# Kernel tuning notes

Measured on AMD Instinct MI355X. Metric: run time of the kernel, lower is better.

The kernel has to match this reference:

```python
import jax, jax.numpy as jnp
import numpy as np

B, L, D, H = 2, 2048, 2048, 16
HD = D // H          # head_dim = 128
LD = HD // 4         # latent_dim = 32


def _linear_params(key, fan_in, fan_out):
    kw, kb = jax.random.split(key)
    bound = 1.0 / np.sqrt(fan_in)
    W = jax.random.uniform(kw, (fan_in, fan_out), jnp.float32, -bound, bound)
    b = jax.random.uniform(kb, (fan_out,), jnp.float32, -bound, bound)
    return W, b


def setup_inputs() -> dict:
    key = jax.random.key(0)
    ks = jax.random.split(key, 12)
    x = jax.random.normal(ks[0], (B, L, D), jnp.float32)
    cos = jax.random.uniform(ks[1], (L, HD // 2), jnp.float32)
    sin = jax.random.uniform(ks[2], (L, HD // 2), jnp.float32)
    Wq, bq = _linear_params(ks[3], D, D)
    Wk, bk = _linear_params(ks[4], D, D)
    Wv, bv = _linear_params(ks[5], D, D)
    Wqc, bqc = _linear_params(ks[6], HD, LD)
    Wkc, bkc = _linear_params(ks[7], HD, LD)
    Wvc, bvc = _linear_params(ks[8], HD, LD)
    Wd, bd = _linear_params(ks[9], LD, HD)
    Wo, bo = _linear_params(ks[10], D, D)
    return dict(x=x, cos=cos, sin=sin, Wq=Wq, bq=bq, Wk=Wk, bk=bk, Wv=Wv, bv=bv,
                Wqc=Wqc, bqc=bqc, Wkc=Wkc, bkc=bkc, Wvc=Wvc, bvc=bvc,
                Wd=Wd, bd=bd, Wo=Wo, bo=bo)


def _apply_rope(q, k, cos, sin):
    # q, k: (B, H, L, HD); cos, sin: (L, HD//2) -> broadcast over B, H
    c = cos[None, None, :, :]
    s = sin[None, None, :, :]
    qe, qo = q[..., ::2], q[..., 1::2]
    ke, ko = k[..., ::2], k[..., 1::2]
    q_rot = jnp.stack([qe * c - qo * s, qe * s + qo * c], axis=-1).reshape(q.shape)
    k_rot = jnp.stack([ke * c - ko * s, ke * s + ko * c], axis=-1).reshape(k.shape)
    return q_rot, k_rot


def reference(x, cos, sin, Wq, bq, Wk, bk, Wv, bv,
              Wqc, bqc, Wkc, bkc, Wvc, bvc, Wd, bd, Wo, bo):
    b, l, d = x.shape
    # projections -> (B, H, L, HD)
    q = (x @ Wq + bq).reshape(b, l, H, HD).transpose(0, 2, 1, 3)
    k = (x @ Wk + bk).reshape(b, l, H, HD).transpose(0, 2, 1, 3)
    v = (x @ Wv + bv).reshape(b, l, H, HD).transpose(0, 2, 1, 3)
    q, k = _apply_rope(q, k, cos, sin)
    # low-rank compression into latent_dim
    qc = jnp.einsum('bhld,de->bhle', q, Wqc) + bqc
    kc = jnp.einsum('bhld,de->bhle', k, Wkc) + bkc
    vc = jnp.einsum('bhld,de->bhle', v, Wvc) + bvc
    scores = jnp.einsum('bhqe,bhke->bhqk', qc, kc) / np.sqrt(LD).astype(np.float32)
    causal = jnp.tril(jnp.ones((l, l), dtype=bool))  # True = keep
    scores = jnp.where(causal[None, None], scores, -jnp.inf)
    probs = jax.nn.softmax(scores, axis=-1)
    attn = jnp.einsum('bhqk,bhke->bhqe', probs, vc)
    attn = jnp.einsum('bhle,ed->bhld', attn, Wd) + bd  # decompress to HD
    attn = attn.transpose(0, 2, 1, 3).reshape(b, l, d)
    return attn @ Wo + bo
```

## Files before the change

### kernel.cpp

```cpp
#include <hip/hip_runtime.h>
#include <hip/hip_bf16.h>


#define Bsz 2
#define Lseq 2048
#define Dmod 2048
#define Hn 16
#define HDim 128
#define LDim 32

typedef __bf16 bf16x8 __attribute__((ext_vector_type(8)));
typedef float f32x4 __attribute__((ext_vector_type(4)));
typedef __hip_bfloat16 bf16;

#define GLDS16(g, l)                                                    \
  __builtin_amdgcn_global_load_lds(                                     \
      (const __attribute__((address_space(1))) unsigned int*)(g),       \
      (__attribute__((address_space(3))) unsigned int*)(l), 16, 0, 0)

#define SM_COS 0
#define SM_SIN 131072
#define SM_WC 262144
#define SM_BC 274432
#define SM_WD 274528
#define SM_BD 278624
#define SM_BO 278752
#define SM_BQKV 280800
#define SM_TOT 286944

__global__ void detect_dtype(const ushort* __restrict__ x, int* __restrict__ flag) {
  int t = threadIdx.x;
  int bad = 0;
  for (int k = 0; k < 4; ++k) {
    ushort u = x[t * 4 + k];
    int ex = (u >> 7) & 0xFF;
    if (ex >= 0xC0) bad = 1;
  }
  unsigned long long b = __ballot(bad);
  if (t == 0) *flag = (b != 0ULL) ? 1 : 0;
}

__device__ inline void conv8(const void* src, size_t so, bf16* dst, size_t dof, int f32) {
  if (f32) {
    const float* s = (const float*)src + so;
    bf16 tmp[8] __attribute__((aligned(16)));
    for (int j = 0; j < 8; ++j) tmp[j] = __float2bfloat16(s[j]);
    *(uint4*)&dst[dof] = *(uint4*)tmp;
  } else {
    *(uint4*)&dst[dof] = *(const uint4*)((const ushort*)src + so);
  }
}

__device__ inline float cv1(const void* s, size_t i, int f32) {
  return f32 ? ((const float*)s)[i] : __bfloat162float(((const bf16*)s)[i]);
}

#define NB_T3 3072
#define NB_WV 2048
#define NB_CX 4096
#define NB_PREP 160
#define NB_FBP 256
#define NB_PREP_ALL (NB_T3 + NB_WV + NB_CX + NB_PREP + NB_FBP)

__global__ __launch_bounds__(256) void prep_all(
    const void* xS, const void* cosS, const void* sinS, const void* WqS,
    const void* WkS, const void* WvS, const void* WoS, const void* WqcS,
    const void* WkcS, const void* WvcS, const void* bqcS, const void* bkcS,
    const void* bvcS, const void* WdS, const void* bdS, const void* boS,
    const void* bqS, const void* bkS, const void* bvS,
    bf16* __restrict__ xb, bf16* __restrict__ WvB, bf16* __restrict__ WtQK,
    bf16* __restrict__ WtO, bf16* __restrict__ small, bf16* __restrict__ wctG,
    bf16* __restrict__ wdtG, float* __restrict__ bo_part,
    const int* __restrict__ flagp) {
  __shared__ __align__(16) char shm[16640];
  int f32 = *flagp;
  int blk = blockIdx.x;
  int t = threadIdx.x;

  if (blk < NB_T3) {
    float (*tile)[65] = (float(*)[65])shm;
    int z = blk >> 10, rem = blk & 1023;
    const void* W = (z == 0) ? WqS : (z == 1) ? WkS : WoS;
    bf16* Wt = (z == 2) ? WtO : (WtQK + (size_t)z * 2048 * 2048);
    int n0 = (rem & 31) * 64, k0 = (rem >> 5) * 64;
    int x = (t & 7) * 8, y = t >> 3;
    for (int p = 0; p < 2; ++p) {
      int r = y + p * 32;
      if (f32) {
        const float* src = (const float*)W + (size_t)(k0 + r) * 2048 + n0 + x;
        float4 a = *(const float4*)src;
        float4 b2 = *(const float4*)(src + 4);
        tile[r][x + 0] = a.x; tile[r][x + 1] = a.y; tile[r][x + 2] = a.z; tile[r][x + 3] = a.w;
        tile[r][x + 4] = b2.x; tile[r][x + 5] = b2.y; tile[r][x + 6] = b2.z; tile[r][x + 7] = b2.w;
      } else {
        const ushort* src = (const ushort*)W + (size_t)(k0 + r) * 2048 + n0 + x;
        uint4 u = *(const uint4*)src;
        bf16* e = (bf16*)&u;
        for (int jj = 0; jj < 8; ++jj) tile[r][x + jj] = __bfloat162float(e[jj]);
      }
    }
    __syncthreads();
    for (int p = 0; p < 2; ++p) {
      int n = y + p * 32;
      bf16 tmp[8] __attribute__((aligned(16)));
      for (int jj = 0; jj < 8; ++jj) tmp[jj] = __float2bfloat16(tile[x + jj][n]);
      *(uint4*)&Wt[(size_t)(n0 + n) * 2048 + k0 + x] = *(uint4*)tmp;
    }
  } else if (blk < NB_T3 + NB_WV) {
    size_t e = ((size_t)(blk - NB_T3) * 256 + t) * 8;
    conv8(WvS, e, WvB, e, f32);
  } else if (blk < NB_T3 + NB_WV + NB_CX) {
    size_t e = ((size_t)(blk - NB_T3 - NB_WV) * 256 + t) * 8;
    conv8(xS, e, xb, e, f32);
  } else if (blk < NB_T3 + NB_WV + NB_CX + NB_PREP) {
    int tid = (blk - NB_T3 - NB_WV - NB_CX) * 256 + t;
    if (tid < SM_TOT / 8) {
      size_t e = (size_t)tid * 8;
      const void* src;
      size_t so;
      if (e < SM_SIN) { src = cosS; so = e - SM_COS; }
      else if (e < SM_WC) { src = sinS; so = e - SM_SIN; }
      else if (e < SM_BC) { size_t r = e - SM_WC; src = (r < 4096) ? WqcS : (r < 8192) ? WkcS : WvcS; so = r & 4095; }
      else if (e < SM_WD) { size_t r = e - SM_BC; src = (r < 32) ? bqcS : (r < 64) ? bkcS : bvcS; so = r & 31; }
      else if (e < SM_BD) { src = WdS; so = e - SM_WD; }
      else if (e < SM_BO) { src = bdS; so = e - SM_BD; }
      else if (e < SM_BQKV) { src = boS; so = e - SM_BO; }
      else { size_t r = e - SM_BQKV; src = (r < 2048) ? bqS : (r < 4096) ? bkS : bvS; so = r & 2047; }
      conv8(src, so, small, e, f32);
    } else {
      int idx = tid - SM_TOT / 8;
      for (int i = idx; i < 16384; i += 40960 - SM_TOT / 8) {
        if (i < 12288) {
          int reg = i >> 12, rem2 = i & 4095, n = rem2 >> 7, k = rem2 & 127;
          const void* src = (reg == 0) ? WqcS : (reg == 1) ? WkcS : WvcS;
          wctG[i] = __float2bfloat16(cv1(src, (size_t)k * 32 + n, f32));
        } else {
          int i2 = i - 12288, o = i2 >> 5, e = i2 & 31;
          wdtG[i2] = __float2bfloat16(cv1(WdS, (size_t)e * 128 + o, f32));
        }
      }
    }
  } else {
    float* red = (float*)shm;
    int rem = blk - (NB_T3 + NB_WV + NB_CX + NB_PREP);
    int nb = rem & 15, kb = rem >> 4;
    int col = nb * 128 + (t & 127);
    int half = t >> 7;
    float s = 0.f;
    int kbase = kb * 128 + half * 64;
    for (int i = 0; i < 64; ++i) {
      int k = kbase + i;
      s += cv1(bdS, k & 127, f32) * cv1(WoS, (size_t)k * 2048 + col, f32);
    }
    red[t] = s;
    __syncthreads();
    if (half == 0) bo_part[kb * 2048 + col] = red[t] + red[t + 128];
  }
}

__global__ __launch_bounds__(256) void fold_all(
    const bf16* __restrict__ WvB, const bf16* __restrict__ wctG,
    const bf16* __restrict__ WtO, const bf16* __restrict__ small,
    const void* boS, const float* __restrict__ bo_part, const void* bvS,
    const void* bvcS, const void* WvcS, bf16* __restrict__ Wvt,
    bf16* __restrict__ Wot, float* __restrict__ boF, float* __restrict__ bvF,
    const int* __restrict__ flagp) {
  int blk = blockIdx.x;
  int t = threadIdx.x, lane = t & 63, w = t >> 6;
  int qd = lane >> 4, ln = lane & 15;
  if (blk < 256) {
    int nb = blk & 15, h = blk >> 4;
    f32x4 acc[2][2] = {};
    for (int kt = 0; kt < 4; ++kt) {
      bf16x8 af[2], bfr[2];
      for (int i = 0; i < 2; ++i)
        af[i] = *(const bf16x8*)&wctG[8192 + (i * 16 + ln) * 128 + kt * 32 + qd * 8];
      for (int j = 0; j < 2; ++j)
        bfr[j] = *(const bf16x8*)&WvB[(size_t)(nb * 128 + w * 32 + j * 16 + ln) * 2048 +
                                      h * 128 + kt * 32 + qd * 8];
      for (int i = 0; i < 2; ++i)
        for (int j = 0; j < 2; ++j)
          acc[i][j] = __builtin_amdgcn_mfma_f32_16x16x32_bf16(af[i], bfr[j], acc[i][j], 0, 0, 0);
    }
    for (int i = 0; i < 2; ++i)
      for (int j = 0; j < 2; ++j)
        for (int r = 0; r < 4; ++r) {
          int e = i * 16 + qd * 4 + r;
          int col = nb * 128 + w * 32 + j * 16 + ln;
          Wvt[(size_t)(h * 32 + e) * 2048 + col] = __float2bfloat16(acc[i][j][r]);
        }
  } else if (blk < 512) {
    int rem = blk - 256;
    int mb = rem & 15, h = rem >> 4;
    f32x4 acc[2][2] = {};
    for (int kt = 0; kt < 4; ++kt) {
      bf16x8 af[2], bfr[2];
      for (int i = 0; i < 2; ++i)
        af[i] = *(const bf16x8*)&WtO[(size_t)(mb * 128 + w * 32 + i * 16 + ln) * 2048 +
                                     h * 128 + kt * 32 + qd * 8];
      for (int j = 0; j < 2; ++j)
        bfr[j] = *(const bf16x8*)&small[SM_WD + (j * 16 + ln) * 128 + kt * 32 + qd * 8];
      for (int i = 0; i < 2; ++i)
        for (int j = 0; j < 2; ++j)
          acc[i][j] = __builtin_amdgcn_mfma_f32_16x16x32_bf16(af[i], bfr[j], acc[i][j], 0, 0, 0);
    }
    for (int i = 0; i < 2; ++i)
      for (int j = 0; j < 2; ++j)
        for (int r = 0; r < 4; ++r) {
          int row = mb * 128 + w * 32 + i * 16 + qd * 4 + r;
          int col = h * 32 + j * 16 + ln;
          Wot[(size_t)row * 512 + col] = __float2bfloat16(acc[i][j][r]);
        }
  } else {
    int f32 = *flagp;
    int tid = (blk - 512) * 256 + t;
    if (tid < 2048) {
      float s = cv1(boS, tid, f32);
      for (int kb = 0; kb < 16; ++kb) s += bo_part[kb * 2048 + tid];
      boF[tid] = s;
    } else if (tid < 2560) {
      int j = tid - 2048, h = j >> 5, e = j & 31;
      float s = cv1(bvcS, e, f32);
      for (int hd = 0; hd < 128; ++hd)
        s += cv1(bvS, h * 128 + hd, f32) * cv1(WvcS, (size_t)hd * 32 + e, f32);
      bvF[j] = s;
    }
  }
}

#define ESTR 136
__global__ __launch_bounds__(256) void gemm_qk_compress(
    const bf16* __restrict__ A, const bf16* __restrict__ Bt,
    const bf16* __restrict__ small, const bf16* __restrict__ wctG,
    bf16* __restrict__ qc, bf16* __restrict__ kc) {
  __shared__ bf16 sh[128 * ESTR];
  bf16* lA = sh;
  bf16* lB = sh + 4096;
  const int K = 2048;
  int id = blockIdx.x;
  int lg = (id & 7) * 128 + (id >> 3);
  int bm = lg >> 5, bn = lg & 31;
  int reg = bn >> 4, h = bn & 15;
  int t = threadIdx.x;
  int lane = t & 63, w = t >> 6;
  int wm = (w >> 1) * 64, wn = (w & 1) * 64;
  int qd = lane >> 4, ln = lane & 15;

  f32x4 acc[4][4] = {};
  const bf16* Ab = A + (size_t)(bm * 128) * K;
  const bf16* Bb = Bt + (size_t)(bn * 128) * K;

  for (int kt = 0; kt < K; kt += 32) {
    for (int p = 0; p < 2; ++p) {
      int slot = t + p * 256;
      int r = slot >> 2, c = (slot & 3) * 8;
      GLDS16(&Ab[(size_t)r * K + kt + c], &lA[slot * 8]);
      GLDS16(&Bb[(size_t)r * K + kt + c], &lB[slot * 8]);
    }
    __syncthreads();
    bf16x8 af[4], bfr[4];
    for (int i = 0; i < 4; ++i) af[i] = *(bf16x8*)&lA[(wm + i * 16 + ln) * 32 + qd * 8];
    for (int j = 0; j < 4; ++j) bfr[j] = *(bf16x8*)&lB[(wn + j * 16 + ln) * 32 + qd * 8];
    for (int i = 0; i < 4; ++i)
      for (int j = 0; j < 4; ++j)
        acc[i][j] = __builtin_amdgcn_mfma_f32_16x16x32_bf16(af[i], bfr[j], acc[i][j], 0, 0, 0);
    __syncthreads();
  }

  for (int j = 0; j < 4; ++j) {
    int col = wn + j * 16 + ln;
    float bv = __bfloat162float(small[SM_BQKV + bn * 128 + col]);
    for (int i = 0; i < 4; ++i)
      for (int r = 0; r < 4; ++r)
        sh[(wm + i * 16 + qd * 4 + r) * ESTR + col] = __float2bfloat16(acc[i][j][r] + bv);
  }
  __syncthreads();

  int r0 = w * 32;
  int b = bm >> 4;
  int bh = b * Hn + h;
  bf16x8 bfr2[2][4];
  for (int nt = 0; nt < 2; ++nt)
    for (int kt = 0; kt < 4; ++kt)
      bfr2[nt][kt] = *(const bf16x8*)&wctG[reg * 4096 + (nt * 16 + ln) * 128 + kt * 32 + qd * 8];
  float bc[2];
  bc[0] = __bfloat162float(small[SM_BC + reg * 32 + ln]);
  bc[1] = __bfloat162float(small[SM_BC + reg * 32 + 16 + ln]);

  for (int mt = 0; mt < 2; ++mt) {
    int lb = r0 + mt * 16 + ln;
    int lg2 = (bm & 15) * 128 + lb;
    f32x4 c2[2] = {};
    for (int kt = 0; kt < 4; ++kt) {
      uint4 u = *(uint4*)&sh[lb * ESTR + kt * 32 + qd * 8];
      bf16* e8 = (bf16*)&u;
      int pbase = kt * 16 + qd * 4;
      for (int j = 0; j < 4; ++j) {
        float cvv = __bfloat162float(small[SM_COS + (size_t)lg2 * 64 + pbase + j]);
        float svv = __bfloat162float(small[SM_SIN + (size_t)lg2 * 64 + pbase + j]);
        float ev = __bfloat162float(e8[2 * j]);
        float ov = __bfloat162float(e8[2 * j + 1]);
        e8[2 * j] = __float2bfloat16(ev * cvv - ov * svv);
        e8[2 * j + 1] = __float2bfloat16(ev * svv + ov * cvv);
      }
      bf16x8 a = *(bf16x8*)&u;
      c2[0] = __builtin_amdgcn_mfma_f32_16x16x32_bf16(a, bfr2[0][kt], c2[0], 0, 0, 0);
      c2[1] = __builtin_amdgcn_mfma_f32_16x16x32_bf16(a, bfr2[1][kt], c2[1], 0, 0, 0);
    }
    int lgbase = (bm & 15) * 128 + r0 + mt * 16 + qd * 4;
    bf16* dst = (reg == 0) ? qc : kc;
    for (int nt = 0; nt < 2; ++nt)
      for (int r = 0; r < 4; ++r)
        dst[((size_t)bh * Lseq + lgbase + r) * 32 + nt * 16 + ln] =
            __float2bfloat16(c2[nt][r] + bc[nt]);
  }
}

__global__ __launch_bounds__(256) void gemm_v_fold(const bf16* __restrict__ A,
                                                   const bf16* __restrict__ Wvt,
                                                   const float* __restrict__ bvF,
                                                   bf16* __restrict__ vcT) {
  __shared__ bf16 lA[64 * 32];
  __shared__ bf16 lB[64 * 32];
  const int K = 2048;
  int bm = blockIdx.y, nb = blockIdx.x;
  int t = threadIdx.x;
  int lane = t & 63, w = t >> 6;
  int wm = (w >> 1) * 32, wn = (w & 1) * 32;
  int qd = lane >> 4, ln = lane & 15;

  f32x4 acc[2][2] = {};
  const bf16* Ab = A + (size_t)(bm * 64) * K;
  const bf16* Bb = Wvt + (size_t)(nb * 64) * K;

  int r = t >> 2, c = (t & 3) * 8;
  for (int kt = 0; kt < K; kt += 32) {
    GLDS16(&Ab[(size_t)r * K + kt + c], &lA[t * 8]);
    GLDS16(&Bb[(size_t)r * K + kt + c], &lB[t * 8]);
    __syncthreads();
    bf16x8 af[2], bfr[2];
    for (int i = 0; i < 2; ++i) af[i] = *(bf16x8*)&lA[(wm + i * 16 + ln) * 32 + qd * 8];
    for (int j = 0; j < 2; ++j) bfr[j] = *(bf16x8*)&lB[(wn + j * 16 + ln) * 32 + qd * 8];
    for (int i = 0; i < 2; ++i)
      for (int j = 0; j < 2; ++j)
        acc[i][j] = __builtin_amdgcn_mfma_f32_16x16x32_bf16(af[i], bfr[j], acc[i][j], 0, 0, 0);
    __syncthreads();
  }

  int b = bm >> 5;
  for (int j = 0; j < 2; ++j) {
    int n = nb * 64 + wn + j * 16 + ln;
    float bb = bvF[n];
    for (int i = 0; i < 2; ++i) {
      int lloc = (bm & 31) * 64 + wm + i * 16 + qd * 4;
      bf16 p4[4] __attribute__((aligned(8)));
      for (int rr = 0; rr < 4; ++rr) p4[rr] = __float2bfloat16(acc[i][j][rr] + bb);
      *(uint2*)&vcT[((size_t)(b * 512 + n)) * 2048 + lloc] = *(uint2*)p4;
    }
  }
}

__global__ __launch_bounds__(256) void gemm_bias_out(const bf16* __restrict__ A,
                                                     const bf16* __restrict__ Bt,
                                                     const float* __restrict__ bias,
                                                     void* __restrict__ C,
                                                     int M, int N, int K,
                                                     const int* __restrict__ flagp) {
  __shared__ bf16 lA[128 * 32];
  __shared__ bf16 lB[128 * 32];
  int f32out = *flagp;
  int bm = blockIdx.y, bn = blockIdx.x;
  int t = threadIdx.x;
  int lane = t & 63, w = t >> 6;
  int wm = (w >> 1) * 64, wn = (w & 1) * 64;
  int qd = lane >> 4, ln = lane & 15;

  f32x4 acc[4][4] = {};
  const bf16* Ab = A + (size_t)(bm * 128) * K;
  const bf16* Bb = Bt + (size_t)(bn * 128) * K;

  for (int kt = 0; kt < K; kt += 32) {
    for (int p = 0; p < 2; ++p) {
      int slot = t + p * 256;
      int r = slot >> 2, c = (slot & 3) * 8;
      GLDS16(&Ab[(size_t)r * K + kt + c], &lA[slot * 8]);
      GLDS16(&Bb[(size_t)r * K + kt + c], &lB[slot * 8]);
    }
    __syncthreads();
    bf16x8 af[4], bfr[4];
    for (int i = 0; i < 4; ++i) af[i] = *(bf16x8*)&lA[(wm + i * 16 + ln) * 32 + qd * 8];
    for (int j = 0; j < 4; ++j) bfr[j] = *(bf16x8*)&lB[(wn + j * 16 + ln) * 32 + qd * 8];
    for (int i = 0; i < 4; ++i)
      for (int j = 0; j < 4; ++j)
        acc[i][j] = __builtin_amdgcn_mfma_f32_16x16x32_bf16(af[i], bfr[j], acc[i][j], 0, 0, 0);
    __syncthreads();
  }
  for (int i = 0; i < 4; ++i)
    for (int j = 0; j < 4; ++j) {
      int col = bn * 128 + wn + j * 16 + ln;
      float bv = bias[col];
      for (int r = 0; r < 4; ++r) {
        int row = bm * 128 + wm + i * 16 + qd * 4 + r;
        float v = acc[i][j][r] + bv;
        if (f32out) ((float*)C)[(size_t)row * N + col] = v;
        else ((bf16*)C)[(size_t)row * N + col] = __float2bfloat16(v);
      }
    }
}

__global__ __launch_bounds__(256) void flash32(const bf16* __restrict__ qc,
                                               const bf16* __restrict__ kc,
                                               const bf16* __restrict__ vcT,
                                               bf16* __restrict__ attn) {
  __shared__ bf16 pbuf[4][16 * 72];
  __shared__ float oL[4][16][33];
  __shared__ float mL[4][16];
  __shared__ float lsL[4][16];
  int t = threadIdx.x;
  int lane = t & 63, w = t >> 6;
  int qd = lane >> 4, ln = lane & 15;
  int blk = blockIdx.x;
  int j = blk & 127;
  int bh = blk >> 7, h = bh & 15, b = bh >> 4;
  int q0 = j * 16;

  bf16x8 qf = *(const bf16x8*)&qc[((size_t)bh * Lseq + q0 + ln) * 32 + qd * 8];

  f32x4 o0 = {}, o1 = {};
  float m[4], ls[4];
  for (int r = 0; r < 4; ++r) { m[r] = -1e30f; ls[r] = 0.f; }
  const float scale = 0.17677669529663687f;

  int n64 = (q0 + 16 + 63) >> 6;
  int nw = (n64 + 3) >> 2;
  int c0 = w * nw;
  int c1 = min(c0 + nw, n64);

  bf16* pb = pbuf[w];
  for (int ci = c0; ci < c1; ++ci) {
    int k0 = ci * 64;
    f32x4 s[4];
    for (int c = 0; c < 4; ++c) {
      bf16x8 kf = *(const bf16x8*)&kc[((size_t)bh * Lseq + k0 + c * 16 + ln) * 32 + qd * 8];
      f32x4 z = {};
      s[c] = __builtin_amdgcn_mfma_f32_16x16x32_bf16(qf, kf, z, 0, 0, 0);
    }
    float sv[4][4], alpha[4];
    for (int r = 0; r < 4; ++r) {
      int qrow = q0 + qd * 4 + r;
      for (int c = 0; c < 4; ++c)
        sv[c][r] = (k0 + c * 16 + ln <= qrow) ? s[c][r] * scale : -1e30f;
    }
    for (int r = 0; r < 4; ++r) {
      float mx = fmaxf(fmaxf(sv[0][r], sv[1][r]), fmaxf(sv[2][r], sv[3][r]));
      for (int off = 1; off < 16; off <<= 1) mx = fmaxf(mx, __shfl_xor(mx, off, 64));
      float mn = fmaxf(m[r], mx);
      alpha[r] = __expf(m[r] - mn);
      m[r] = mn;
      float rs = 0.f;
      for (int c = 0; c < 4; ++c) { sv[c][r] = __expf(sv[c][r] - mn); rs += sv[c][r]; }
      ls[r] = ls[r] * alpha[r] + rs;
      o0[r] *= alpha[r];
      o1[r] *= alpha[r];
    }
    for (int r = 0; r < 4; ++r)
      for (int c = 0; c < 4; ++c)
        pb[(qd * 4 + r) * 72 + c * 16 + ln] = __float2bfloat16(sv[c][r]);
    asm volatile("s_waitcnt lgkmcnt(0)" ::: "memory");
    bf16x8 pf0 = *(bf16x8*)&pb[ln * 72 + qd * 8];
    bf16x8 pf1 = *(bf16x8*)&pb[ln * 72 + 32 + qd * 8];
    bf16x8 vf00 = *(const bf16x8*)&vcT[((size_t)bh * 32 + ln) * Lseq + k0 + qd * 8];
    bf16x8 vf01 = *(const bf16x8*)&vcT[((size_t)bh * 32 + ln) * Lseq + k0 + 32 + qd * 8];
    bf16x8 vf10 = *(const bf16x8*)&vcT[((size_t)bh * 32 + 16 + ln) * Lseq + k0 + qd * 8];
    bf16x8 vf11 = *(const bf16x8*)&vcT[((size_t)bh * 32 + 16 + ln) * Lseq + k0 + 32 + qd * 8];
    o0 = __builtin_amdgcn_mfma_f32_16x16x32_bf16(pf0, vf00, o0, 0, 0, 0);
    o0 = __builtin_amdgcn_mfma_f32_16x16x32_bf16(pf1, vf01, o0, 0, 0, 0);
    o1 = __builtin_amdgcn_mfma_f32_16x16x32_bf16(pf0, vf10, o1, 0, 0, 0);
    o1 = __builtin_amdgcn_mfma_f32_16x16x32_bf16(pf1, vf11, o1, 0, 0, 0);
  }

  for (int r = 0; r < 4; ++r)
    for (int off = 1; off < 16; off <<= 1) ls[r] += __shfl_xor(ls[r], off, 64);

  for (int r = 0; r < 4; ++r) {
    int row = qd * 4 + r;
    oL[w][row][ln] = o0[r];
    oL[w][row][16 + ln] = o1[r];
    if (ln == 0) { mL[w][row] = m[r]; lsL[w][row] = ls[r]; }
  }
  __syncthreads();

  for (int idx = t; idx < 512; idx += 256) {
    int row = idx >> 5, col = idx & 31;
    float m0 = mL[0][row], m1 = mL[1][row], m2 = mL[2][row], m3 = mL[3][row];
    float ms = fmaxf(fmaxf(m0, m1), fmaxf(m2, m3));
    float e0 = __expf(m0 - ms), e1 = __expf(m1 - ms);
    float e2 = __expf(m2 - ms), e3 = __expf(m3 - ms);
    float lsum = lsL[0][row] * e0 + lsL[1][row] * e1 + lsL[2][row] * e2 + lsL[3][row] * e3;
    float val = oL[0][row][col] * e0 + oL[1][row][col] * e1 +
                oL[2][row][col] * e2 + oL[3][row][col] * e3;
    int l = q0 + row;
    attn[((size_t)(b * Lseq + l)) * 512 + h * 32 + col] = __float2bfloat16(val / lsum);
  }
}

extern "C" void kernel_launch(void* const* d_in, const int* in_sizes, int n_in,
                              void* d_out, int out_size, void* d_ws, size_t ws_size,
                              hipStream_t stream) {
  const void* x = d_in[0];
  const void* cosS = d_in[1];
  const void* sinS = d_in[2];
  const void* Wq = d_in[3];
  const void* bq = d_in[4];
  const void* Wk = d_in[5];
  const void* bk = d_in[6];
  const void* Wv = d_in[7];
  const void* bv = d_in[8];
  const void* Wqc = d_in[9];
  const void* bqc = d_in[10];
  const void* Wkc = d_in[11];
  const void* bkc = d_in[12];
  const void* Wvc = d_in[13];
  const void* bvc = d_in[14];
  const void* Wd = d_in[15];
  const void* bd = d_in[16];
  const void* Wo = d_in[17];
  const void* bo = d_in[18];

  char* ws = (char*)d_ws;
  size_t off = 0;
  auto alloc = [&](size_t bytes) {
    char* p = ws + off;
    off += (bytes + 255) & ~(size_t)255;
    return p;
  };
  int* flag = (int*)alloc(256);
  bf16* small = (bf16*)alloc((size_t)SM_TOT * 2);
  bf16* wctG = (bf16*)alloc((size_t)12288 * 2);
  bf16* wdtG = (bf16*)alloc((size_t)4096 * 2);
  bf16* xb = (bf16*)alloc((size_t)4096 * 2048 * 2);
  bf16* WvB = (bf16*)alloc((size_t)2048 * 2048 * 2);
  bf16* WtQK = (bf16*)alloc((size_t)4096 * 2048 * 2);
  bf16* WtO = (bf16*)alloc((size_t)2048 * 2048 * 2);
  bf16* Wvt = (bf16*)alloc((size_t)512 * 2048 * 2);
  bf16* Wot = (bf16*)alloc((size_t)2048 * 512 * 2);
  float* bo_part = (float*)alloc((size_t)16 * 2048 * 4);
  float* boF = (float*)alloc((size_t)2048 * 4);
  float* bvF = (float*)alloc((size_t)512 * 4);
  bf16* qcW = (bf16*)alloc((size_t)65536 * 32 * 2);
  bf16* kcW = (bf16*)alloc((size_t)65536 * 32 * 2);
  bf16* vcTW = (bf16*)alloc((size_t)65536 * 32 * 2);
  bf16* attnW = (bf16*)alloc((size_t)4096 * 512 * 2);

  dim3 tb(256);
  detect_dtype<<<1, 64, 0, stream>>>((const ushort*)x, flag);
  prep_all<<<NB_PREP_ALL, tb, 0, stream>>>(
      x, cosS, sinS, Wq, Wk, Wv, Wo, Wqc, Wkc, Wvc, bqc, bkc, bvc, Wd, bd, bo,
      bq, bk, bv, xb, WvB, WtQK, WtO, small, wctG, wdtG, bo_part, flag);
  fold_all<<<522, tb, 0, stream>>>(WvB, wctG, WtO, small, bo, bo_part, bv, bvc,
                                   Wvc, Wvt, Wot, boF, bvF, flag);
  gemm_qk_compress<<<1024, tb, 0, stream>>>(xb, WtQK, small, wctG, qcW, kcW);
  gemm_v_fold<<<dim3(8, 64), tb, 0, stream>>>(xb, Wvt, bvF, vcTW);
  flash32<<<4096, tb, 0, stream>>>(qcW, kcW, vcTW, attnW);
  gemm_bias_out<<<dim3(16, 32), tb, 0, stream>>>(attnW, Wot, boF, d_out, 4096, 2048,
                                                 512, flag);
}
```

Baseline: 409.1 us.

## Merge QK and V GEMMs into one launch; prefetch K/V and use exp2 in flash

The QK compress GEMM and the V fold GEMM are combined into a single kernel launch, with a block-index split between the two paths, so the smaller V work can fill the tail of the larger grid. The QK block mapping drops the earlier swizzle in favour of a plain row-major order, and the RoPE cos/sin values are now read with one vector load each. In the flash attention kernel the next K tile is loaded one iteration ahead, the V loads are issued before the softmax, and the exponentials use exp2f with log2(e) folded into the scale. Dropping the swizzle may reduce L2 reuse of the weight tiles, and a 1536-block grid that mixes two tile shapes may not balance well.

```diff
diff --git a/kernel.cpp b/kernel.cpp
--- a/kernel.cpp
+++ b/kernel.cpp
@@ -229,133 +229,132 @@
 }
 
 #define ESTR 136
-__global__ __launch_bounds__(256) void gemm_qk_compress(
+__global__ __launch_bounds__(256) void gemm_qkv(
     const bf16* __restrict__ A, const bf16* __restrict__ Bt,
-    const bf16* __restrict__ small, const bf16* __restrict__ wctG,
-    bf16* __restrict__ qc, bf16* __restrict__ kc) {
+    const bf16* __restrict__ Wvt, const bf16* __restrict__ small,
+    const bf16* __restrict__ wctG, const float* __restrict__ bvF,
+    bf16* __restrict__ qc, bf16* __restrict__ kc, bf16* __restrict__ vcT) {
   __shared__ bf16 sh[128 * ESTR];
-  bf16* lA = sh;
-  bf16* lB = sh + 4096;
   const int K = 2048;
   int id = blockIdx.x;
-  int lg = (id & 7) * 128 + (id >> 3);
-  int bm = lg >> 5, bn = lg & 31;
-  int reg = bn >> 4, h = bn & 15;
   int t = threadIdx.x;
   int lane = t & 63, w = t >> 6;
-  int wm = (w >> 1) * 64, wn = (w & 1) * 64;
   int qd = lane >> 4, ln = lane & 15;
 
-  f32x4 acc[4][4] = {};
-  const bf16* Ab = A + (size_t)(bm * 128) * K;
-  const bf16* Bb = Bt + (size_t)(bn * 128) * K;
-
-  for (int kt = 0; kt < K; kt += 32) {
-    for (int p = 0; p < 2; ++p) {
-      int slot = t + p * 256;
-      int r = slot >> 2, c = (slot & 3) * 8;
-      GLDS16(&Ab[(size_t)r * K + kt + c], &lA[slot * 8]);
-      GLDS16(&Bb[(size_t)r * K + kt + c], &lB[slot * 8]);
+  if (id < 1024) {
+    bf16* lA = sh;
+    bf16* lB = sh + 4096;
+    int bn = id & 31, bm = id >> 5;
+    int reg = bn >> 4, h = bn & 15;
+    int wm = (w >> 1) * 64, wn = (w & 1) * 64;
+
+    f32x4 acc[4][4] = {};
+    const bf16* Ab = A + (size_t)(bm * 128) * K;
+    const bf16* Bb = Bt + (size_t)(bn * 128) * K;
+
+    for (int kt = 0; kt < K; kt += 32) {
+      for (int p = 0; p < 2; ++p) {
+        int slot = t + p * 256;
+        int r = slot >> 2, c = (slot & 3) * 8;
+        GLDS16(&Ab[(size_t)r * K + kt + c], &lA[slot * 8]);
+        GLDS16(&Bb[(size_t)r * K + kt + c], &lB[slot * 8]);
+      }
+      __syncthreads();
+      bf16x8 af[4], bfr[4];
+      for (int i = 0; i < 4; ++i) af[i] = *(bf16x8*)&lA[(wm + i * 16 + ln) * 32 + qd * 8];
+      for (int j = 0; j < 4; ++j) bfr[j] = *(bf16x8*)&lB[(wn + j * 16 + ln) * 32 + qd * 8];
+      for (int i = 0; i < 4; ++i)
+        for (int j = 0; j < 4; ++j)
+          acc[i][j] = __builtin_amdgcn_mfma_f32_16x16x32_bf16(af[i], bfr[j], acc[i][j], 0, 0, 0);
+      __syncthreads();
+    }
+
+    for (int j = 0; j < 4; ++j) {
+      int col = wn + j * 16 + ln;
+      float bv = __bfloat162float(small[SM_BQKV + bn * 128 + col]);
+      for (int i = 0; i < 4; ++i)
+        for (int r = 0; r < 4; ++r)
+          sh[(wm + i * 16 + qd * 4 + r) * ESTR + col] = __float2bfloat16(acc[i][j][r] + bv);
     }
     __syncthreads();
-    bf16x8 af[4], bfr[4];
-    for (int i = 0; i < 4; ++i) af[i] = *(bf16x8*)&lA[(wm + i * 16 + ln) * 32 + qd * 8];
-    for (int j = 0; j < 4; ++j) bfr[j] = *(bf16x8*)&lB[(wn + j * 16 + ln) * 32 + qd * 8];
-    for (int i = 0; i < 4; ++i)
-      for (int j = 0; j < 4; ++j)
-        acc[i][j] = __builtin_amdgcn_mfma_f32_16x16x32_bf16(af[i], bfr[j], acc[i][j], 0, 0, 0);
-    __syncthreads();
-  }
-
-  for (int j = 0; j < 4; ++j) {
-    int col = wn + j * 16 + ln;
-    float bv = __bfloat162float(small[SM_BQKV + bn * 128 + col]);
-    for (int i = 0; i < 4; ++i)
-      for (int r = 0; r < 4; ++r)
-        sh[(wm + i * 16 + qd * 4 + r) * ESTR + col] = __float2bfloat16(acc[i][j][r] + bv);
-  }
-  __syncthreads();
-
-  int r0 = w * 32;
-  int b = bm >> 4;
-  int bh = b * Hn + h;
-  bf16x8 bfr2[2][4];
-  for (int nt = 0; nt < 2; ++nt)
-    for (int kt = 0; kt < 4; ++kt)
-      bfr2[nt][kt] = *(const bf16x8*)&wctG[reg * 4096 + (nt * 16 + ln) * 128 + kt * 32 + qd * 8];
-  float bc[2];
-  bc[0] = __bfloat162float(small[SM_BC + reg * 32 + ln]);
-  bc[1] = __bfloat162float(small[SM_BC + reg * 32 + 16 + ln]);
-
-  for (int mt = 0; mt < 2; ++mt) {
-    int lb = r0 + mt * 16 + ln;
-    int lg2 = (bm & 15) * 128 + lb;
-    f32x4 c2[2] = {};
-    for (int kt = 0; kt < 4; ++kt) {
-      uint4 u = *(uint4*)&sh[lb * ESTR + kt * 32 + qd * 8];
-      bf16* e8 = (bf16*)&u;
-      int pbase = kt * 16 + qd * 4;
-      for (int j = 0; j < 4; ++j) {
-        float cvv = __bfloat162float(small[SM_COS + (size_t)lg2 * 64 + pbase + j]);
-        float svv = __bfloat162float(small[SM_SIN + (size_t)lg2 * 64 + pbase + j]);
-        float ev = __bfloat162float(e8[2 * j]);
-        float ov = __bfloat162float(e8[2 * j + 1]);
-        e8[2 * j] = __float2bfloat16(ev * cvv - ov * svv);
-        e8[2 * j + 1] = __float2bfloat16(ev * svv + ov * cvv);
+
+    int r0 = w * 32;
+    int b = bm >> 4;
+    int bh = b * Hn + h;
+    bf16x8 bfr2[2][4];
+    for (int nt = 0; nt < 2; ++nt)
+      for (int kt = 0; kt < 4; ++kt)
+        bfr2[nt][kt] = *(const bf16x8*)&wctG[reg * 4096 + (nt * 16 + ln) * 128 + kt * 32 + qd * 8];
+    float bc[2];
+    bc[0] = __bfloat162float(small[SM_BC + reg * 32 + ln]);
+    bc[1] = __bfloat162float(small[SM_BC + reg * 32 + 16 + ln]);
+
+    for (int mt = 0; mt < 2; ++mt) {
+      int lb = r0 + mt * 16 + ln;
+      int lg2 = (bm & 15) * 128 + lb;
+      f32x4 c2[2] = {};
+      for (int kt = 0; kt < 4; ++kt) {
+        uint4 u = *(uint4*)&sh[lb * ESTR + kt * 32 + qd * 8];
+        bf16* e8 = (bf16*)&u;
+        int pbase = kt * 16 + qd * 4;
+        uint2 cu = *(const uint2*)&small[SM_COS + (size_t)lg2 * 64 + pbase];
+        uint2 su = *(const uint2*)&small[SM_SIN + (size_t)lg2 * 64 + pbase];
+        const bf16* cp = (const bf16*)&cu;
+        const bf16* sp = (const bf16*)&su;
+        for (int j = 0; j < 4; ++j) {
+          float cvv = __bfloat162float(cp[j]);
+          float svv = __bfloat162float(sp[j]);
+          float ev = __bfloat162float(e8[2 * j]);
+          float ov = __bfloat162float(e8[2 * j + 1]);
+          e8[2 * j] = __float2bfloat16(ev * cvv - ov * svv);
+          e8[2 * j + 1] = __float2bfloat16(ev * svv + ov * cvv);
+        }
+        bf16x8 a = *(bf16x8*)&u;
+        c2[0] = __builtin_amdgcn_mfma_f32_16x16x32_bf16(a, bfr2[0][kt], c2[0], 0, 0, 0);
+        c2[1] = __builtin_amdgcn_mfma_f32_16x16x32_bf16(a, bfr2[1][kt], c2[1], 0, 0, 0);
       }
-      bf16x8 a = *(bf16x8*)&u;
-      c2[0] = __builtin_amdgcn_mfma_f32_16x16x32_bf16(a, bfr2[0][kt], c2[0], 0, 0, 0);
-      c2[1] = __builtin_amdgcn_mfma_f32_16x16x32_bf16(a, bfr2[1][kt], c2[1], 0, 0, 0);
-    }
-    int lgbase = (bm & 15) * 128 + r0 + mt * 16 + qd * 4;
-    bf16* dst = (reg == 0) ? qc : kc;
-    for (int nt = 0; nt < 2; ++nt)
-      for (int r = 0; r < 4; ++r)
-        dst[((size_t)bh * Lseq + lgbase + r) * 32 + nt * 16 + ln] =
-            __float2bfloat16(c2[nt][r] + bc[nt]);
-  }
-}
-
-__global__ __launch_bounds__(256) void gemm_v_fold(const bf16* __restrict__ A,
-                                                   const bf16* __restrict__ Wvt,
-                                                   const float* __restrict__ bvF,
-                                                   bf16* __restrict__ vcT) {
-  __shared__ bf16 lA[64 * 32];
-  __shared__ bf16 lB[64 * 32];
-  const int K = 2048;
-  int bm = blockIdx.y, nb = blockIdx.x;
-  int t = threadIdx.x;
-  int lane = t & 63, w = t >> 6;
-  int wm = (w >> 1) * 32, wn = (w & 1) * 32;
-  int qd = lane >> 4, ln = lane & 15;
-
-  f32x4 acc[2][2] = {};
-  const bf16* Ab = A + (size_t)(bm * 64) * K;
-  const bf16* Bb = Wvt + (size_t)(nb * 64) * K;
-
-  int r = t >> 2, c = (t & 3) * 8;
-  for (int kt = 0; kt < K; kt += 32) {
-    GLDS16(&Ab[(size_t)r * K + kt + c], &lA[t * 8]);
-    GLDS16(&Bb[(size_t)r * K + kt + c], &lB[t * 8]);
-    __syncthreads();
-    bf16x8 af[2], bfr[2];
-    for (int i = 0; i < 2; ++i) af[i] = *(bf16x8*)&lA[(wm + i * 16 + ln) * 32 + qd * 8];
-    for (int j = 0; j < 2; ++j) bfr[j] = *(bf16x8*)&lB[(wn + j * 16 + ln) * 32 + qd * 8];
-    for (int i = 0; i < 2; ++i)
-      for (int j = 0; j < 2; ++j)
-        acc[i][j] = __builtin_amdgcn_mfma_f32_16x16x32_bf16(af[i], bfr[j], acc[i][j], 0, 0, 0);
-    __syncthreads();
-  }
-
-  int b = bm >> 5;
-  for (int j = 0; j < 2; ++j) {
-    int n = nb * 64 + wn + j * 16 + ln;
-    float bb = bvF[n];
-    for (int i = 0; i < 2; ++i) {
-      int lloc = (bm & 31) * 64 + wm + i * 16 + qd * 4;
-      bf16 p4[4] __attribute__((aligned(8)));
-      for (int rr = 0; rr < 4; ++rr) p4[rr] = __float2bfloat16(acc[i][j][rr] + bb);
-      *(uint2*)&vcT[((size_t)(b * 512 + n)) * 2048 + lloc] = *(uint2*)p4;
+      int lgbase = (bm & 15) * 128 + r0 + mt * 16 + qd * 4;
+      bf16* dst = (reg == 0) ? qc : kc;
+      for (int nt = 0; nt < 2; ++nt)
+        for (int r = 0; r < 4; ++r)
+          dst[((size_t)bh * Lseq + lgbase + r) * 32 + nt * 16 + ln] =
+              __float2bfloat16(c2[nt][r] + bc[nt]);
+    }
+  } else {
+    bf16* lA = sh;
+    bf16* lB = sh + 2048;
+    int rem = id - 1024;
+    int nb = rem & 7, bm = rem >> 3;
+    int wm = (w >> 1) * 32, wn = (w & 1) * 32;
+
+    f32x4 acc[2][2] = {};
+    const bf16* Ab = A + (size_t)(bm * 64) * K;
+    const bf16* Bb = Wvt + (size_t)(nb * 64) * K;
+
+    int r = t >> 2, c = (t & 3) * 8;
+    for (int kt = 0; kt < K; kt += 32) {
+      GLDS16(&Ab[(size_t)r * K + kt + c], &lA[t * 8]);
+      GLDS16(&Bb[(size_t)r * K + kt + c], &lB[t * 8]);
+      __syncthreads();
+      bf16x8 af[2], bfr[2];
+      for (int i = 0; i < 2; ++i) af[i] = *(bf16x8*)&lA[(wm + i * 16 + ln) * 32 + qd * 8];
+      for (int j = 0; j < 2; ++j) bfr[j] = *(bf16x8*)&lB[(wn + j * 16 + ln) * 32 + qd * 8];
+      for (int i = 0; i < 2; ++i)
+        for (int j = 0; j < 2; ++j)
+          acc[i][j] = __builtin_amdgcn_mfma_f32_16x16x32_bf16(af[i], bfr[j], acc[i][j], 0, 0, 0);
+      __syncthreads();
+    }
+
+    int b = bm >> 5;
+    for (int j = 0; j < 2; ++j) {
+      int n = nb * 64 + wn + j * 16 + ln;
+      float bb = bvF[n];
+      for (int i = 0; i < 2; ++i) {
+        int lloc = (bm & 31) * 64 + wm + i * 16 + qd * 4;
+        bf16 p4[4] __attribute__((aligned(8)));
+        for (int rr = 0; rr < 4; ++rr) p4[rr] = __float2bfloat16(acc[i][j][rr] + bb);
+        *(uint2*)&vcT[((size_t)(b * 512 + n)) * 2048 + lloc] = *(uint2*)p4;
+      }
     }
   }
 }
@@ -429,7 +428,7 @@
   f32x4 o0 = {}, o1 = {};
   float m[4], ls[4];
   for (int r = 0; r < 4; ++r) { m[r] = -1e30f; ls[r] = 0.f; }
-  const float scale = 0.17677669529663687f;
+  const float scale2 = 0.17677669529663687f * 1.4426950408889634f;
 
   int n64 = (q0 + 16 + 63) >> 6;
   int nw = (n64 + 3) >> 2;
@@ -437,28 +436,43 @@
   int c1 = min(c0 + nw, n64);
 
   bf16* pb = pbuf[w];
+  bf16x8 kf[4];
+  if (c0 < c1) {
+    int k0 = c0 * 64;
+    for (int c = 0; c < 4; ++c)
+      kf[c] = *(const bf16x8*)&kc[((size_t)bh * Lseq + k0 + c * 16 + ln) * 32 + qd * 8];
+  }
   for (int ci = c0; ci < c1; ++ci) {
     int k0 = ci * 64;
     f32x4 s[4];
     for (int c = 0; c < 4; ++c) {
-      bf16x8 kf = *(const bf16x8*)&kc[((size_t)bh * Lseq + k0 + c * 16 + ln) * 32 + qd * 8];
       f32x4 z = {};
-      s[c] = __builtin_amdgcn_mfma_f32_16x16x32_bf16(qf, kf, z, 0, 0, 0);
+      s[c] = __builtin_amdgcn_mfma_f32_16x16x32_bf16(qf, kf[c], z, 0, 0, 0);
+    }
+    size_t vbase = ((size_t)bh * 32 + ln) * Lseq + k0 + qd * 8;
+    bf16x8 vf00 = *(const bf16x8*)&vcT[vbase];
+    bf16x8 vf01 = *(const bf16x8*)&vcT[vbase + 32];
+    bf16x8 vf10 = *(const bf16x8*)&vcT[vbase + (size_t)16 * Lseq];
+    bf16x8 vf11 = *(const bf16x8*)&vcT[vbase + (size_t)16 * Lseq + 32];
+    if (ci + 1 < c1) {
+      int k0n = k0 + 64;
+      for (int c = 0; c < 4; ++c)
+        kf[c] = *(const bf16x8*)&kc[((size_t)bh * Lseq + k0n + c * 16 + ln) * 32 + qd * 8];
     }
     float sv[4][4], alpha[4];
     for (int r = 0; r < 4; ++r) {
       int qrow = q0 + qd * 4 + r;
       for (int c = 0; c < 4; ++c)
-        sv[c][r] = (k0 + c * 16 + ln <= qrow) ? s[c][r] * scale : -1e30f;
+        sv[c][r] = (k0 + c * 16 + ln <= qrow) ? s[c][r] * scale2 : -1e30f;
     }
     for (int r = 0; r < 4; ++r) {
       float mx = fmaxf(fmaxf(sv[0][r], sv[1][r]), fmaxf(sv[2][r], sv[3][r]));
       for (int off = 1; off < 16; off <<= 1) mx = fmaxf(mx, __shfl_xor(mx, off, 64));
       float mn = fmaxf(m[r], mx);
-      alpha[r] = __expf(m[r] - mn);
+      alpha[r] = exp2f(m[r] - mn);
       m[r] = mn;
       float rs = 0.f;
-      for (int c = 0; c < 4; ++c) { sv[c][r] = __expf(sv[c][r] - mn); rs += sv[c][r]; }
+      for (int c = 0; c < 4; ++c) { sv[c][r] = exp2f(sv[c][r] - mn); rs += sv[c][r]; }
       ls[r] = ls[r] * alpha[r] + rs;
       o0[r] *= alpha[r];
       o1[r] *= alpha[r];
@@ -469,10 +483,6 @@
     asm volatile("s_waitcnt lgkmcnt(0)" ::: "memory");
     bf16x8 pf0 = *(bf16x8*)&pb[ln * 72 + qd * 8];
     bf16x8 pf1 = *(bf16x8*)&pb[ln * 72 + 32 + qd * 8];
-    bf16x8 vf00 = *(const bf16x8*)&vcT[((size_t)bh * 32 + ln) * Lseq + k0 + qd * 8];
-    bf16x8 vf01 = *(const bf16x8*)&vcT[((size_t)bh * 32 + ln) * Lseq + k0 + 32 + qd * 8];
-    bf16x8 vf10 = *(const bf16x8*)&vcT[((size_t)bh * 32 + 16 + ln) * Lseq + k0 + qd * 8];
-    bf16x8 vf11 = *(const bf16x8*)&vcT[((size_t)bh * 32 + 16 + ln) * Lseq + k0 + 32 + qd * 8];
     o0 = __builtin_amdgcn_mfma_f32_16x16x32_bf16(pf0, vf00, o0, 0, 0, 0);
     o0 = __builtin_amdgcn_mfma_f32_16x16x32_bf16(pf1, vf01, o0, 0, 0, 0);
     o1 = __builtin_amdgcn_mfma_f32_16x16x32_bf16(pf0, vf10, o1, 0, 0, 0);
@@ -494,8 +504,8 @@
     int row = idx >> 5, col = idx & 31;
     float m0 = mL[0][row], m1 = mL[1][row], m2 = mL[2][row], m3 = mL[3][row];
     float ms = fmaxf(fmaxf(m0, m1), fmaxf(m2, m3));
-    float e0 = __expf(m0 - ms), e1 = __expf(m1 - ms);
-    float e2 = __expf(m2 - ms), e3 = __expf(m3 - ms);
+    float e0 = exp2f(m0 - ms), e1 = exp2f(m1 - ms);
+    float e2 = exp2f(m2 - ms), e3 = exp2f(m3 - ms);
     float lsum = lsL[0][row] * e0 + lsL[1][row] * e1 + lsL[2][row] * e2 + lsL[3][row] * e3;
     float val = oL[0][row][col] * e0 + oL[1][row][col] * e1 +
                 oL[2][row][col] * e2 + oL[3][row][col] * e3;
@@ -559,8 +569,7 @@
       bq, bk, bv, xb, WvB, WtQK, WtO, small, wctG, wdtG, bo_part, flag);
   fold_all<<<522, tb, 0, stream>>>(WvB, wctG, WtO, small, bo, bo_part, bv, bvc,
                                    Wvc, Wvt, Wot, boF, bvF, flag);
-  gemm_qk_compress<<<1024, tb, 0, stream>>>(xb, WtQK, small, wctG, qcW, kcW);
-  gemm_v_fold<<<dim3(8, 64), tb, 0, stream>>>(xb, Wvt, bvF, vcTW);
+  gemm_qkv<<<1536, tb, 0, stream>>>(xb, WtQK, Wvt, small, wctG, bvF, qcW, kcW, vcTW);
   flash32<<<4096, tb, 0, stream>>>(qcW, kcW, vcTW, attnW);
   gemm_bias_out<<<dim3(16, 32), tb, 0, stream>>>(attnW, Wot, boF, d_out, 4096, 2048,
                                                  512, flag);
```

Result: faster. 394.2 us (-3.6%).
